# Kernel tuning notes

Measured on AMD Instinct MI355X. Metric: run time of the kernel, lower is better.

## Reference

```python
import jax, jax.numpy as jnp
import numpy as np

H = 70  # hidden size == input size


def _renorm_rows(w, max_norm=1.0, eps=1e-7):
    # emulate nn.Embedding(max_norm=1.0): clip row L2 norm to <= 1
    n = jnp.linalg.norm(w, axis=-1, keepdims=True)
    return jnp.where(n > max_norm, w * (max_norm / (n + eps)), w)


def _lstm(x, w_ih, w_hh, b_ih, b_hh):
    # x: (B, T, H). PyTorch gate order: i, f, g, o.
    B = x.shape[0]
    xg = jnp.einsum('bth,gh->btg', x, w_ih) + (b_ih + b_hh)  # (B, T, 4H)
    def step(carry, xt):
        h, c = carry
        gates = xt + h @ w_hh.T  # (B, 4H)
        i, f, g, o = jnp.split(gates, 4, axis=-1)
        i = jax.nn.sigmoid(i); f = jax.nn.sigmoid(f)
        g = jnp.tanh(g); o = jax.nn.sigmoid(o)
        c = f * c + i * g
        h = o * jnp.tanh(c)
        return (h, c), h
    h0 = jnp.zeros((B, H), x.dtype)
    (_, _), hs = jax.lax.scan(step, (h0, h0), jnp.swapaxes(xg, 0, 1))
    return jnp.swapaxes(hs, 0, 1)  # (B, T, H)


def setup_inputs() -> dict:
    key = jax.random.key(0)
    ks = jax.random.split(key, 12)
    B, S, C = 128, 512, 1104
    s = 0.1
    return {
        'x': jax.random.uniform(ks[0], (B, S, C), jnp.float32),
        'embed_w': jax.random.normal(ks[1], (C, H), jnp.float32),
        'w_ih': jax.random.normal(ks[2], (4 * H, H), jnp.float32) * s,
        'w_hh': jax.random.normal(ks[3], (4 * H, H), jnp.float32) * s,
        'b_ih': jax.random.normal(ks[4], (4 * H,), jnp.float32) * s,
        'b_hh': jax.random.normal(ks[5], (4 * H,), jnp.float32) * s,
        'attn_w1': jax.random.normal(ks[6], (64, H), jnp.float32) * s,
        'attn_b1': jax.random.normal(ks[7], (64,), jnp.float32) * s,
        'attn_w2': jax.random.normal(ks[8], (1, 64), jnp.float32) * s,
        'attn_b2': jax.random.normal(ks[9], (1,), jnp.float32) * s,
        'fc_w': jax.random.normal(ks[10], (3, H), jnp.float32) * s,
        'fc_b': jax.random.normal(ks[11], (3,), jnp.float32) * s,
    }


def reference(x, embed_w, w_ih, w_hh, b_ih, b_hh, attn_w1, attn_b1, attn_w2, attn_b2, fc_w, fc_b):
    w = _renorm_rows(embed_w)                      # (C, H)
    # fused form of (x[...,None] * weight).sum(dim=2): plain GEMM
    e = jnp.einsum('bsc,ch->bsh', x, w)            # (B, S, H)
    out = _lstm(e, w_ih, w_hh, b_ih, b_hh)         # (B, S, H)
    # self-attention pooling
    energy = jax.nn.relu(out @ attn_w1.T + attn_b1) @ attn_w2.T + attn_b2  # (B,S,1)
    weights = jax.nn.softmax(energy[..., 0], axis=1)                        # (B,S)
    pooled = jnp.einsum('bsh,bs->bh', out, weights)                         # (B,H)
    # dropout is identity at eval
    logits = pooled @ fc_w.T + fc_b
    return jax.nn.softmax(logits, axis=1)
```

## Files before the change

kernel.cpp:

```cpp
#include <hip/hip_runtime.h>
#include <math.h>

#define HDIM 70
#define HPAD 72
#define GATES 280
#define NG 288
#define TLEN 512
#define BATCH 128
#define CDIM 1104
#define KW 1152
#define ROWS 65536

#define OFF_WRN   0
#define OFF_BIAS  77312
#define OFF_WCT   77632
#define OFF_XG    243520
#define OFF_HOUT  9418560
#define OFF_EN    14137152

typedef short short8 __attribute__((ext_vector_type(8)));
typedef float f32x4 __attribute__((ext_vector_type(4)));

__device__ __forceinline__ unsigned short f2bf(float f) {
    unsigned int u = __float_as_uint(f);
    u = (u + 0x7fffu + ((u >> 16) & 1u)) >> 16;
    return (unsigned short)u;
}
__device__ __forceinline__ float bf2f(unsigned short s) {
    return __uint_as_float(((unsigned int)s) << 16);
}

__global__ __launch_bounds__(64) void k_renorm(const float* __restrict__ w,
                                               float* __restrict__ wrn) {
    const int row = blockIdx.x;
    const int lane = threadIdx.x;
    const float* wr = w + row * HDIM;
    float v0 = wr[lane];
    float v1 = (lane < 6) ? wr[64 + lane] : 0.0f;
    float ss = v0 * v0 + v1 * v1;
    #pragma unroll
    for (int off = 32; off > 0; off >>= 1) ss += __shfl_down(ss, off);
    float tot = __shfl(ss, 0);
    float n = sqrtf(tot);
    float scale = (n > 1.0f) ? 1.0f / (n + 1e-7f) : 1.0f;
    wrn[row * HDIM + lane] = v0 * scale;
    if (lane < 6) wrn[row * HDIM + 64 + lane] = v1 * scale;
}

__global__ __launch_bounds__(256) void k_prep(const float* __restrict__ wrn,
                                              const float* __restrict__ w_ih,
                                              const float* __restrict__ b_ih,
                                              const float* __restrict__ b_hh,
                                              unsigned short* __restrict__ wcT,
                                              float* __restrict__ bias) {
    const int n = blockIdx.x;
    const int tid = threadIdx.x;
    float wr[HDIM];
    if (n < GATES) {
        #pragma unroll
        for (int h = 0; h < HDIM; ++h) wr[h] = w_ih[n * HDIM + h];
        if (tid == 0) bias[n] = b_ih[n] + b_hh[n];
    } else {
        #pragma unroll
        for (int h = 0; h < HDIM; ++h) wr[h] = 0.0f;
    }
    for (int c = tid; c < KW; c += 256) {
        float a = 0.0f;
        if (n < GATES && c < CDIM) {
            const float* wc = wrn + c * HDIM;
            #pragma unroll
            for (int h = 0; h < HDIM; ++h) a += wr[h] * wc[h];
        }
        wcT[(size_t)n * KW + c] = f2bf(a);
    }
}

__global__ __launch_bounds__(256, 2) void k_xg_gemm(const float* __restrict__ x,
                                                    const unsigned short* __restrict__ wcT,
                                                    const float* __restrict__ bias,
                                                    unsigned short* __restrict__ xg) {
    __shared__ __align__(16) unsigned short A_lds[128 * 72];
    __shared__ __align__(16) unsigned short B_lds[NG * 72];
    const int tid = threadIdx.x;
    const int lane = tid & 63;
    const int w = tid >> 6;
    const int mh = (w >> 1) * 64;
    const int nh = (w & 1) * 144;
    const int l15 = lane & 15;
    const int q = lane >> 4;
    const size_t rbase = (size_t)blockIdx.x * 128;

    f32x4 acc[4][9];
    #pragma unroll
    for (int mt = 0; mt < 4; ++mt)
        #pragma unroll
        for (int nt = 0; nt < 9; ++nt) acc[mt][nt] = (f32x4){0.f, 0.f, 0.f, 0.f};

    const int r_st = tid >> 1;
    const int kh_st = (tid & 1) * 32;

    for (int kc = 0; kc < 18; ++kc) {
        const int k0 = kc * 64;
        {
            const float* xr = x + (rbase + r_st) * (size_t)CDIM + k0 + kh_st;
            unsigned short* dst = &A_lds[r_st * 72 + kh_st];
            #pragma unroll
            for (int qq = 0; qq < 8; ++qq) {
                const int kk = k0 + kh_st + qq * 4;
                float4 v = make_float4(0.f, 0.f, 0.f, 0.f);
                if (kk < CDIM) v = *(const float4*)(xr + qq * 4);
                unsigned int lo = (unsigned int)f2bf(v.x) | ((unsigned int)f2bf(v.y) << 16);
                unsigned int hi = (unsigned int)f2bf(v.z) | ((unsigned int)f2bf(v.w) << 16);
                uint2 pv; pv.x = lo; pv.y = hi;
                *(uint2*)&dst[qq * 4] = pv;
            }
        }
        {
            #pragma unroll
            for (int p = 0; p < 9; ++p) {
                const int cid = tid + p * 256;
                const int n = cid >> 3;
                const int ko = (cid & 7) * 8;
                uint4 v = *(const uint4*)(wcT + (size_t)n * KW + k0 + ko);
                *(uint4*)&B_lds[n * 72 + ko] = v;
            }
        }
        __syncthreads();
        #pragma unroll
        for (int ks = 0; ks < 2; ++ks) {
            short8 a[4];
            short8 bfr[9];
            #pragma unroll
            for (int mt = 0; mt < 4; ++mt)
                a[mt] = *(const short8*)&A_lds[(mh + mt * 16 + l15) * 72 + ks * 32 + q * 8];
            #pragma unroll
            for (int nt = 0; nt < 9; ++nt)
                bfr[nt] = *(const short8*)&B_lds[(nh + nt * 16 + l15) * 72 + ks * 32 + q * 8];
            #pragma unroll
            for (int mt = 0; mt < 4; ++mt)
                #pragma unroll
                for (int nt = 0; nt < 9; ++nt)
                    acc[mt][nt] = __builtin_amdgcn_mfma_f32_16x16x32_bf16(a[mt], bfr[nt], acc[mt][nt], 0, 0, 0);
        }
        __syncthreads();
    }
    #pragma unroll
    for (int nt = 0; nt < 9; ++nt) {
        const int n_g = nh + nt * 16 + l15;
        if (n_g >= GATES) continue;
        const float bv = bias[n_g];
        #pragma unroll
        for (int mt = 0; mt < 4; ++mt) {
            #pragma unroll
            for (int r = 0; r < 4; ++r) {
                const size_t row = rbase + mh + mt * 16 + q * 4 + r;
                xg[row * GATES + n_g] = f2bf(acc[mt][nt][r] + bv);
            }
        }
    }
}

__device__ __forceinline__ float tanh_fast(float v) {
    v = fminf(fmaxf(v, -20.0f), 20.0f);
    float E = __expf(2.0f * v);
    return (E - 1.0f) / (E + 1.0f);
}
__device__ __forceinline__ float sigmoid_fast(float v) {
    return 1.0f / (1.0f + __expf(-v));
}

#define PF 8
__global__ __launch_bounds__(320) void k_lstm(const unsigned short* __restrict__ xg,
                                              const float* __restrict__ w_hh,
                                              float* __restrict__ hout) {
    __shared__ __align__(16) float h_lds[HPAD];
    __shared__ float gates_lds[GATES];
    const int tid = threadIdx.x;
    const int b = blockIdx.x;
    float whh[HPAD];
    if (tid < GATES) {
        #pragma unroll
        for (int j = 0; j < HDIM; ++j) whh[j] = w_hh[tid * HDIM + j];
        whh[70] = whh[71] = 0.0f;
    } else {
        #pragma unroll
        for (int j = 0; j < HPAD; ++j) whh[j] = 0.0f;
    }
    if (tid < HPAD) h_lds[tid] = 0.0f;
    float c_reg = 0.0f;

    const unsigned short* xp = xg + (size_t)b * TLEN * GATES + (tid < GATES ? tid : 0);
    float xbuf[PF];
    #pragma unroll
    for (int i = 0; i < PF; ++i) xbuf[i] = bf2f(xp[i * GATES]);
    __syncthreads();

    #pragma unroll 8
    for (int t = 0; t < TLEN; ++t) {
        const int slot = t & (PF - 1);
        const float xcur = xbuf[slot];
        xbuf[slot] = bf2f(xp[((t + PF) & (TLEN - 1)) * GATES]);
        float a0 = 0.f, a1 = 0.f, a2 = 0.f, a3 = 0.f;
        #pragma unroll
        for (int jj = 0; jj < 18; ++jj) {
            float4 hv = ((const float4*)h_lds)[jj];
            a0 += hv.x * whh[4 * jj];
            a1 += hv.y * whh[4 * jj + 1];
            a2 += hv.z * whh[4 * jj + 2];
            a3 += hv.w * whh[4 * jj + 3];
        }
        const float acc = xcur + ((a0 + a1) + (a2 + a3));
        if (tid < GATES) {
            float a;
            if (tid < 140)      a = sigmoid_fast(acc);
            else if (tid < 210) a = tanh_fast(acc);
            else                a = sigmoid_fast(acc);
            gates_lds[tid] = a;
        }
        __syncthreads();
        if (tid < HDIM) {
            const float iv = gates_lds[tid];
            const float fv = gates_lds[tid + 70];
            const float gv = gates_lds[tid + 140];
            const float ov = gates_lds[tid + 210];
            c_reg = fv * c_reg + iv * gv;
            const float hn = ov * tanh_fast(c_reg);
            h_lds[tid] = hn;
            hout[((size_t)b * TLEN + t) * HPAD + tid] = hn;
        }
        __syncthreads();
    }
}

__global__ __launch_bounds__(256) void k_energy(const float* __restrict__ hout,
                                                const float* __restrict__ w1,
                                                const float* __restrict__ b1,
                                                const float* __restrict__ w2,
                                                const float* __restrict__ b2,
                                                float* __restrict__ energy) {
    const int lane = threadIdx.x & 63;
    const int wid = blockIdx.x * 4 + (threadIdx.x >> 6);
    float w1r[HPAD];
    #pragma unroll
    for (int c = 0; c < HDIM; ++c) w1r[c] = w1[lane * HDIM + c];
    w1r[70] = w1r[71] = 0.0f;
    const float b1v = b1[lane];
    const float w2v = w2[lane];
    const float b2v = b2[0];
    for (int row = wid; row < ROWS; row += 4096) {
        const float4* rp = (const float4*)(hout + (size_t)row * HPAD);
        float a0 = 0.f, a1 = 0.f, a2 = 0.f, a3 = 0.f;
        #pragma unroll
        for (int jj = 0; jj < 18; ++jj) {
            float4 v = rp[jj];
            a0 += v.x * w1r[4 * jj];
            a1 += v.y * w1r[4 * jj + 1];
            a2 += v.z * w1r[4 * jj + 2];
            a3 += v.w * w1r[4 * jj + 3];
        }
        float hid = fmaxf((a0 + a1) + (a2 + a3) + b1v, 0.0f) * w2v;
        #pragma unroll
        for (int off = 32; off > 0; off >>= 1) hid += __shfl_down(hid, off);
        if (lane == 0) energy[row] = hid + b2v;
    }
}

__global__ __launch_bounds__(128) void k_pool(const float* __restrict__ hout,
                                              const float* __restrict__ energy,
                                              const float* __restrict__ fc_w,
                                              const float* __restrict__ fc_b,
                                              float* __restrict__ outp) {
    __shared__ float red[128];
    __shared__ float wexp[TLEN];
    __shared__ float pooledL[HDIM];
    const int tid = threadIdx.x;
    const int b = blockIdx.x;
    float v[4];
    #pragma unroll
    for (int k = 0; k < 4; ++k) v[k] = energy[b * TLEN + tid + 128 * k];
    float m = fmaxf(fmaxf(v[0], v[1]), fmaxf(v[2], v[3]));
    red[tid] = m; __syncthreads();
    for (int s = 64; s > 0; s >>= 1) {
        if (tid < s) red[tid] = fmaxf(red[tid], red[tid + s]);
        __syncthreads();
    }
    const float M = red[0]; __syncthreads();
    float s4 = 0.f;
    #pragma unroll
    for (int k = 0; k < 4; ++k) {
        float ex = __expf(v[k] - M);
        wexp[tid + 128 * k] = ex;
        s4 += ex;
    }
    red[tid] = s4; __syncthreads();
    for (int s = 64; s > 0; s >>= 1) {
        if (tid < s) red[tid] += red[tid + s];
        __syncthreads();
    }
    const float rinv = 1.0f / red[0];
    if (tid < HDIM) {
        float a0 = 0.f, a1 = 0.f, a2 = 0.f, a3 = 0.f;
        const float* hp = hout + (size_t)b * TLEN * HPAD + tid;
        for (int s = 0; s < TLEN; s += 4) {
            a0 += wexp[s]     * hp[(size_t)(s)     * HPAD];
            a1 += wexp[s + 1] * hp[(size_t)(s + 1) * HPAD];
            a2 += wexp[s + 2] * hp[(size_t)(s + 2) * HPAD];
            a3 += wexp[s + 3] * hp[(size_t)(s + 3) * HPAD];
        }
        pooledL[tid] = ((a0 + a1) + (a2 + a3)) * rinv;
    }
    __syncthreads();
    if (tid == 0) {
        float l[3];
        #pragma unroll
        for (int i = 0; i < 3; ++i) {
            float a = fc_b[i];
            for (int h = 0; h < HDIM; ++h) a += fc_w[i * HDIM + h] * pooledL[h];
            l[i] = a;
        }
        float m3 = fmaxf(l[0], fmaxf(l[1], l[2]));
        float e0 = __expf(l[0] - m3), e1 = __expf(l[1] - m3), e2 = __expf(l[2] - m3);
        float rs = 1.0f / (e0 + e1 + e2);
        outp[b * 3 + 0] = e0 * rs;
        outp[b * 3 + 1] = e1 * rs;
        outp[b * 3 + 2] = e2 * rs;
    }
}

extern "C" void kernel_launch(void* const* d_in, const int* in_sizes, int n_in,
                              void* d_out, int out_size, void* d_ws, size_t ws_size,
                              hipStream_t stream) {
    const float* x       = (const float*)d_in[0];
    const float* embed_w = (const float*)d_in[1];
    const float* w_ih    = (const float*)d_in[2];
    const float* w_hh    = (const float*)d_in[3];
    const float* b_ih    = (const float*)d_in[4];
    const float* b_hh    = (const float*)d_in[5];
    const float* aw1     = (const float*)d_in[6];
    const float* ab1     = (const float*)d_in[7];
    const float* aw2     = (const float*)d_in[8];
    const float* ab2     = (const float*)d_in[9];
    const float* fc_w    = (const float*)d_in[10];
    const float* fc_b    = (const float*)d_in[11];
    float* outp = (float*)d_out;
    float* ws = (float*)d_ws;

    float* wrn  = ws + OFF_WRN;
    float* bias = ws + OFF_BIAS;
    unsigned short* wcT = (unsigned short*)(ws + OFF_WCT);
    unsigned short* xgp = (unsigned short*)(ws + OFF_XG);
    float* ho = ws + OFF_HOUT;
    float* en = ws + OFF_EN;

    k_renorm<<<CDIM, 64, 0, stream>>>(embed_w, wrn);
    k_prep<<<NG, 256, 0, stream>>>(wrn, w_ih, b_ih, b_hh, wcT, bias);
    k_xg_gemm<<<512, 256, 0, stream>>>(x, wcT, bias, xgp);
    k_lstm<<<BATCH, 320, 0, stream>>>(xgp, w_hh, ho);
    k_energy<<<1024, 256, 0, stream>>>(ho, aw1, ab1, aw2, ab2, en);
    k_pool<<<BATCH, 128, 0, stream>>>(ho, en, fc_w, fc_b, outp);
}
```

Baseline: 861.9 us.

## Batch 16 sequences per LSTM block using MFMA recurrence and LDS ring prefetch

```diff
diff --git a/kernel.cpp b/kernel.cpp
--- a/kernel.cpp
+++ b/kernel.cpp
@@ -17,6 +17,7 @@
 #define OFF_XG    243520
 #define OFF_HOUT  9418560
 #define OFF_EN    14137152
+#define OFF_WHH   0
 
 typedef short short8 __attribute__((ext_vector_type(8)));
 typedef float f32x4 __attribute__((ext_vector_type(4)));
@@ -73,6 +74,16 @@
         }
         wcT[(size_t)n * KW + c] = f2bf(a);
     }
+}
+
+__global__ __launch_bounds__(96) void k_prep_whh(const float* __restrict__ w_hh,
+                                                 unsigned short* __restrict__ whh) {
+    const int rrow = blockIdx.x;
+    const int k = threadIdx.x;
+    const int g = rrow / 80;
+    const int j = rrow % 80;
+    float v = (j < HDIM && k < HDIM) ? w_hh[(size_t)(g * HDIM + j) * HDIM + k] : 0.0f;
+    whh[(size_t)rrow * 96 + k] = f2bf(v);
 }
 
 __global__ __launch_bounds__(256, 2) void k_xg_gemm(const float* __restrict__ x,
@@ -154,81 +165,136 @@
             #pragma unroll
             for (int r = 0; r < 4; ++r) {
                 const size_t row = rbase + mh + mt * 16 + q * 4 + r;
-                xg[row * GATES + n_g] = f2bf(acc[mt][nt][r] + bv);
-            }
-        }
-    }
-}
-
-__device__ __forceinline__ float tanh_fast(float v) {
-    v = fminf(fmaxf(v, -20.0f), 20.0f);
-    float E = __expf(2.0f * v);
-    return (E - 1.0f) / (E + 1.0f);
-}
+                const int bb = (int)(row >> 9);
+                const int tt = (int)(row & 511);
+                xg[((size_t)((bb >> 4) * 512 + tt) * 16 + (bb & 15)) * GATES + n_g] =
+                    f2bf(acc[mt][nt][r] + bv);
+            }
+        }
+    }
+}
+
 __device__ __forceinline__ float sigmoid_fast(float v) {
     return 1.0f / (1.0f + __expf(-v));
 }
 
-#define PF 8
-__global__ __launch_bounds__(320) void k_lstm(const unsigned short* __restrict__ xg,
-                                              const float* __restrict__ w_hh,
-                                              float* __restrict__ hout) {
-    __shared__ __align__(16) float h_lds[HPAD];
-    __shared__ float gates_lds[GATES];
+#define RSLOT 4496
+
+__global__ __launch_bounds__(384, 1) void k_lstm(const unsigned short* __restrict__ xg,
+                                                 const unsigned short* __restrict__ whh,
+                                                 float* __restrict__ hout) {
+    __shared__ __align__(16) unsigned short Hb[2][16 * 104];
+    __shared__ __align__(16) unsigned short ring[4][RSLOT];
     const int tid = threadIdx.x;
-    const int b = blockIdx.x;
-    float whh[HPAD];
-    if (tid < GATES) {
-        #pragma unroll
-        for (int j = 0; j < HDIM; ++j) whh[j] = w_hh[tid * HDIM + j];
-        whh[70] = whh[71] = 0.0f;
+    const int b8 = blockIdx.x;
+    const int wv = tid >> 6;
+    const int l = tid & 63;
+    const int l15 = l & 15;
+    const int q = l >> 4;
+    const unsigned short* xgb = xg + (size_t)b8 * TLEN * 16 * GATES;
+
+    for (int i = tid; i < 16 * 104; i += 384) ((unsigned int*)Hb)[i] = 0u;
+
+    short8 afr[4][3];
+    uint4 r0[9], r1[9];
+    if (wv < 5) {
+        #pragma unroll
+        for (int g = 0; g < 4; ++g)
+            #pragma unroll
+            for (int ks = 0; ks < 3; ++ks)
+                afr[g][ks] = *(const short8*)&whh[(size_t)((5 * g + wv) * 16 + l15) * 96 + ks * 32 + q * 8];
     } else {
         #pragma unroll
-        for (int j = 0; j < HPAD; ++j) whh[j] = 0.0f;
-    }
-    if (tid < HPAD) h_lds[tid] = 0.0f;
-    float c_reg = 0.0f;
-
-    const unsigned short* xp = xg + (size_t)b * TLEN * GATES + (tid < GATES ? tid : 0);
-    float xbuf[PF];
-    #pragma unroll
-    for (int i = 0; i < PF; ++i) xbuf[i] = bf2f(xp[i * GATES]);
+        for (int s = 0; s < 2; ++s)
+            for (int c = l; c < 560; c += 64)
+                *(uint4*)&ring[s][c * 8] = *(const uint4*)(xgb + (size_t)s * 16 * GATES + c * 8);
+        #pragma unroll
+        for (int i = 0; i < 9; ++i) {
+            const int c = l + i * 64;
+            if (c < 560) {
+                r0[i] = *(const uint4*)(xgb + (size_t)2 * 16 * GATES + c * 8);
+                r1[i] = *(const uint4*)(xgb + (size_t)3 * 16 * GATES + c * 8);
+            }
+        }
+    }
+    const int jb = wv * 16 + q * 4;
+    float creg[4] = {0.f, 0.f, 0.f, 0.f};
     __syncthreads();
 
-    #pragma unroll 8
+    #pragma unroll 4
     for (int t = 0; t < TLEN; ++t) {
-        const int slot = t & (PF - 1);
-        const float xcur = xbuf[slot];
-        xbuf[slot] = bf2f(xp[((t + PF) & (TLEN - 1)) * GATES]);
-        float a0 = 0.f, a1 = 0.f, a2 = 0.f, a3 = 0.f;
-        #pragma unroll
-        for (int jj = 0; jj < 18; ++jj) {
-            float4 hv = ((const float4*)h_lds)[jj];
-            a0 += hv.x * whh[4 * jj];
-            a1 += hv.y * whh[4 * jj + 1];
-            a2 += hv.z * whh[4 * jj + 2];
-            a3 += hv.w * whh[4 * jj + 3];
-        }
-        const float acc = xcur + ((a0 + a1) + (a2 + a3));
-        if (tid < GATES) {
-            float a;
-            if (tid < 140)      a = sigmoid_fast(acc);
-            else if (tid < 210) a = tanh_fast(acc);
-            else                a = sigmoid_fast(acc);
-            gates_lds[tid] = a;
-        }
-        __syncthreads();
-        if (tid < HDIM) {
-            const float iv = gates_lds[tid];
-            const float fv = gates_lds[tid + 70];
-            const float gv = gates_lds[tid + 140];
-            const float ov = gates_lds[tid + 210];
-            c_reg = fv * c_reg + iv * gv;
-            const float hn = ov * tanh_fast(c_reg);
-            h_lds[tid] = hn;
-            hout[((size_t)b * TLEN + t) * HPAD + tid] = hn;
-        }
-        __syncthreads();
+        if (wv < 5) {
+            const unsigned short* rg = &ring[t & 3][l15 * GATES];
+            float u[4][4];
+            #pragma unroll
+            for (int g = 0; g < 4; ++g) {
+                const int base = g * 70 + jb;
+                const unsigned int w0 = *(const unsigned int*)&rg[base];
+                const unsigned int w1 = *(const unsigned int*)&rg[base + 2];
+                u[g][0] = bf2f((unsigned short)(w0 & 0xffffu));
+                u[g][1] = bf2f((unsigned short)(w0 >> 16));
+                u[g][2] = bf2f((unsigned short)(w1 & 0xffffu));
+                u[g][3] = bf2f((unsigned short)(w1 >> 16));
+            }
+            const unsigned short* hb = &Hb[t & 1][l15 * 104];
+            f32x4 acc[4];
+            #pragma unroll
+            for (int g = 0; g < 4; ++g) acc[g] = (f32x4){0.f, 0.f, 0.f, 0.f};
+            #pragma unroll
+            for (int ks = 0; ks < 3; ++ks) {
+                const short8 bfr = *(const short8*)&hb[ks * 32 + q * 8];
+                #pragma unroll
+                for (int g = 0; g < 4; ++g)
+                    acc[g] = __builtin_amdgcn_mfma_f32_16x16x32_bf16(afr[g][ks], bfr, acc[g], 0, 0, 0);
+            }
+            float h[4];
+            #pragma unroll
+            for (int r = 0; r < 4; ++r) {
+                const float iv = sigmoid_fast(acc[0][r] + u[0][r]);
+                const float fv = sigmoid_fast(acc[1][r] + u[1][r]);
+                const float gv = fmaf(2.f, sigmoid_fast(2.f * (acc[2][r] + u[2][r])), -1.f);
+                const float ov = sigmoid_fast(acc[3][r] + u[3][r]);
+                creg[r] = fmaf(fv, creg[r], iv * gv);
+                const float hv = ov * fmaf(2.f, sigmoid_fast(2.f * creg[r]), -1.f);
+                h[r] = (jb + r < HDIM) ? hv : 0.f;
+            }
+            uint2 pp;
+            pp.x = (unsigned int)f2bf(h[0]) | ((unsigned int)f2bf(h[1]) << 16);
+            pp.y = (unsigned int)f2bf(h[2]) | ((unsigned int)f2bf(h[3]) << 16);
+            *(uint2*)&Hb[(t + 1) & 1][l15 * 104 + jb] = pp;
+            float* hop = hout + ((size_t)(b8 * 16 + l15) * TLEN + t) * HPAD + jb;
+            if (jb + 3 < HDIM) {
+                *(float4*)hop = make_float4(h[0], h[1], h[2], h[3]);
+            } else if (jb < HDIM) {
+                hop[0] = h[0]; hop[1] = h[1];
+            }
+        } else {
+            uint4* dst = (uint4*)&ring[(t + 2) & 3][0];
+            if ((t & 1) == 0) {
+                if (t + 2 < TLEN) {
+                    #pragma unroll
+                    for (int i = 0; i < 9; ++i) { const int c = l + i * 64; if (c < 560) dst[c] = r0[i]; }
+                }
+                if (t + 4 < TLEN) {
+                    const unsigned short* src = xgb + (size_t)(t + 4) * 16 * GATES;
+                    #pragma unroll
+                    for (int i = 0; i < 9; ++i) { const int c = l + i * 64; if (c < 560) r0[i] = *(const uint4*)(src + c * 8); }
+                }
+            } else {
+                if (t + 2 < TLEN) {
+                    #pragma unroll
+                    for (int i = 0; i < 9; ++i) { const int c = l + i * 64; if (c < 560) dst[c] = r1[i]; }
+                }
+                if (t + 4 < TLEN) {
+                    const unsigned short* src = xgb + (size_t)(t + 4) * 16 * GATES;
+                    #pragma unroll
+                    for (int i = 0; i < 9; ++i) { const int c = l + i * 64; if (c < 560) r1[i] = *(const uint4*)(src + c * 8); }
+                }
+            }
+        }
+        asm volatile("s_waitcnt lgkmcnt(0)" ::: "memory");
+        __builtin_amdgcn_s_barrier();
+        __builtin_amdgcn_sched_barrier(0);
     }
 }
 
@@ -347,15 +413,17 @@
 
     float* wrn  = ws + OFF_WRN;
     float* bias = ws + OFF_BIAS;
-    unsigned short* wcT = (unsigned short*)(ws + OFF_WCT);
-    unsigned short* xgp = (unsigned short*)(ws + OFF_XG);
+    unsigned short* wcT  = (unsigned short*)(ws + OFF_WCT);
+    unsigned short* xgp  = (unsigned short*)(ws + OFF_XG);
+    unsigned short* whhp = (unsigned short*)(ws + OFF_WHH);
     float* ho = ws + OFF_HOUT;
     float* en = ws + OFF_EN;
 
     k_renorm<<<CDIM, 64, 0, stream>>>(embed_w, wrn);
     k_prep<<<NG, 256, 0, stream>>>(wrn, w_ih, b_ih, b_hh, wcT, bias);
+    k_prep_whh<<<320, 96, 0, stream>>>(w_hh, whhp);
     k_xg_gemm<<<512, 256, 0, stream>>>(x, wcT, bias, xgp);
-    k_lstm<<<BATCH, 320, 0, stream>>>(xgp, w_hh, ho);
+    k_lstm<<<8, 384, 0, stream>>>(xgp, whhp, ho);
     k_energy<<<1024, 256, 0, stream>>>(ho, aw1, ab1, aw2, ab2, en);
     k_pool<<<BATCH, 128, 0, stream>>>(ho, en, fc_w, fc_b, outp);
 }
```

Measured after the change: 1.337 ms. 1.55x slower.
